# Kernel tuning notes

Measured on AMD Instinct MI355X. Metric: run time of the kernel, lower is better.

## Reference

```python
import jax, jax.numpy as jnp
import numpy as np

# dims: batch, nodes, d_node, d_edge, d_attn_hid, heads, d_node_hid, d_edge_hid, layers
B, N, DN, DE, DH, H, DNH, DEH, L = 2, 256, 128, 64, 128, 8, 512, 256, 2
DHH = DH // H  # per-head dim
SCALE = 1.0 / (DH ** 0.5)  # source scales by full d_hid, not per-head dim


def _ln(x, g, b):
    m = jnp.mean(x, -1, keepdims=True)
    v = jnp.mean((x - m) ** 2, -1, keepdims=True)
    return (x - m) * jax.lax.rsqrt(v + 1e-5) * g + b


def _gelu(x):
    return jax.nn.gelu(x, approximate=False)  # torch nn.GELU default = exact erf


def setup_inputs() -> dict:
    key = jax.random.key(0)
    ks = iter(jax.random.split(key, 40))
    def w(shape, scale=0.02):
        return jax.random.normal(next(ks), shape, jnp.float32) * scale
    return {
        "node_features": jax.random.normal(next(ks), (B, N, DN), jnp.float32),
        "edge_features": jax.random.normal(next(ks), (B, N, N, DE), jnp.float32),
        "Wqkv_n": w((L, DN, 3 * DH)),
        "Wqkv_e": w((L, DE, 4 * DH)),
        "Wo": w((L, DH, DN)), "bo": jnp.zeros((L, DN), jnp.float32),
        "Wl0": w((L, DN, DN)), "bl0": jnp.zeros((L, DN), jnp.float32),
        "ln0_g": jnp.ones((L, DN), jnp.float32), "ln0_b": jnp.zeros((L, DN), jnp.float32),
        "Wm1": w((L, DN, DNH)), "Wm2": w((L, DNH, DN)), "bm2": jnp.zeros((L, DN), jnp.float32),
        "ln1_g": jnp.ones((L, DN), jnp.float32), "ln1_b": jnp.zeros((L, DN), jnp.float32),
        "We0": w((L, 2 * DE, DEH)), "be0": jnp.zeros((L, DEH), jnp.float32),
        "Ws": w((L, DN, DEH)), "bs": jnp.zeros((L, DEH), jnp.float32),
        "Wt": w((L, DN, DEH)), "bt": jnp.zeros((L, DEH), jnp.float32),
        "We1": w((L, DEH, DE)), "be1": jnp.zeros((L, DE), jnp.float32),
        "eln0_g": jnp.ones((L, DE), jnp.float32), "eln0_b": jnp.zeros((L, DE), jnp.float32),
        "Wem1": w((L, DE, DEH)), "Wem2": w((L, DEH, DE)), "bem2": jnp.zeros((L, DE), jnp.float32),
        "eln1_g": jnp.ones((L, DE), jnp.float32), "eln1_b": jnp.zeros((L, DE), jnp.float32),
    }


def _forward(node_features, edge_features, Wqkv_n, Wqkv_e, Wo, bo, Wl0, bl0,
             ln0_g, ln0_b, Wm1, Wm2, bm2, ln1_g, ln1_b, We0, be0, Ws, bs, Wt, bt,
             We1, be1, eln0_g, eln0_b, Wem1, Wem2, bem2, eln1_g, eln1_b):
    x, e = node_features, edge_features
    for l in range(L):
        # --- RTAttention (modulate_v=True, eval mode) ---
        qkv_n = (x @ Wqkv_n[l]).reshape(B, N, H, 3 * DHH).transpose(0, 2, 1, 3)  # b h n 3d
        qn, kn, vn = jnp.split(qkv_n, 3, axis=-1)
        qkv_e = (e @ Wqkv_e[l]).reshape(B, N, N, H, 4 * DHH).transpose(0, 3, 1, 2, 4)  # b h i j 4d
        eq, ek, ev, em = jnp.split(qkv_e, 4, axis=-1)
        q = qn[:, :, :, None, :] + eq            # b h i j d
        k = kn[:, :, None, :, :] + ek            # b h i j d
        v = vn[:, :, None, :, :] * em + ev       # modulated values
        dots = SCALE * jnp.einsum('bhijd,bhijd->bhij', q, k)
        attn = jax.nn.softmax(dots, axis=-1)
        out = jnp.einsum('bhij,bhijd->bhid', attn, v)
        out = out.transpose(0, 2, 1, 3).reshape(B, N, DH)
        attn_out = out @ Wo[l] + bo[l]
        # --- node updates: ln(x + lin0(attn)); ln(x + mlp(x)) ---
        x = _ln(x + (attn_out @ Wl0[l] + bl0[l]), ln0_g[l], ln0_b[l])
        x = _ln(x + (_gelu(x @ Wm1[l]) @ Wm2[l] + bm2[l]), ln1_g[l], ln1_b[l])
        # --- edge updates (EdgeLayer) ---
        src = (x @ Ws[l] + bs[l])[:, :, None, :]   # broadcast over target j
        tgt = (x @ Wt[l] + bt[l])[:, None, :, :]   # broadcast over source i
        ecat = jnp.concatenate([e, e.transpose(0, 2, 1, 3)], axis=-1)  # [e_ij, e_ji]
        h = _gelu(ecat @ We0[l] + be0[l] + src + tgt)
        e = _ln(e + (h @ We1[l] + be1[l]), eln0_g[l], eln0_b[l])
        e = _ln(e + (_gelu(e @ Wem1[l]) @ Wem2[l] + bem2[l]), eln1_g[l], eln1_b[l])
    return x, e


def reference(node_features, edge_features, Wqkv_n, Wqkv_e, Wo, bo, Wl0, bl0,
              ln0_g, ln0_b, Wm1, Wm2, bm2, ln1_g, ln1_b, We0, be0, Ws, bs, Wt, bt,
              We1, be1, eln0_g, eln0_b, Wem1, Wem2, bem2, eln1_g, eln1_b):
    return _forward(node_features, edge_features, Wqkv_n, Wqkv_e, Wo, bo, Wl0, bl0,
                    ln0_g, ln0_b, Wm1, Wm2, bm2, ln1_g, ln1_b, We0, be0, Ws, bs, Wt, bt,
                    We1, be1, eln0_g, eln0_b, Wem1, Wem2, bem2, eln1_g, eln1_b)
```

## Files before the change

### kernel.cpp

```cpp
#include <hip/hip_runtime.h>
#include <hip/hip_bf16.h>
#include <stdint.h>

#define BB 2
#define NN 256
#define DN 128
#define DE 64
#define DH 128
#define NH 8
#define DHH 16
#define DNH 512
#define DEH 256
#define NL 2
#define SCALE_ATT 0.08838834764831845f

typedef __hip_bfloat16 bf16;
typedef __attribute__((ext_vector_type(8))) short short8;
typedef __attribute__((ext_vector_type(4))) float f32x4;

__device__ __forceinline__ float gelu_f(float x) {
  return 0.5f * x * (1.0f + erff(x * 0.70710678118654752f));
}
__device__ __forceinline__ float gelu_t(float x) {
  float m2u = x * fmaf(x * x, -0.07135481627f, -1.59576912161f);
  float e = __expf(m2u);
  return x * __builtin_amdgcn_rcpf(1.f + e);
}

template <int ctrl>
__device__ __forceinline__ float dppf(float v) {
  return __int_as_float(
      __builtin_amdgcn_update_dpp(0, __float_as_int(v), ctrl, 0xF, 0xF, true));
}
__device__ __forceinline__ float row_sum16(float v) {
  v += dppf<0xB1>(v);
  v += dppf<0x4E>(v);
  v += dppf<0x124>(v);
  v += dppf<0x128>(v);
  return v;
}
__device__ __forceinline__ float row_max16(float v) {
  v = fmaxf(v, dppf<0xB1>(v));
  v = fmaxf(v, dppf<0x4E>(v));
  v = fmaxf(v, dppf<0x124>(v));
  v = fmaxf(v, dppf<0x128>(v));
  return v;
}
__device__ __forceinline__ float wave_sum(float v) {
  v = row_sum16(v);
  v += __shfl_xor(v, 16, 64);
  v += __shfl_xor(v, 32, 64);
  return v;
}
__device__ __forceinline__ float wave_max(float v) {
  v = row_max16(v);
  v = fmaxf(v, __shfl_xor(v, 16, 64));
  v = fmaxf(v, __shfl_xor(v, 32, 64));
  return v;
}

__device__ __forceinline__ short f2bf(float f) {
  union { float f; uint32_t u; } v{f};
  uint32_t r = (v.u + 0x7FFFu + ((v.u >> 16) & 1u)) >> 16;
  return (short)r;
}
__device__ __forceinline__ float bf2f(short s) {
  union { uint32_t u; float f; } v;
  v.u = ((uint32_t)(uint16_t)s) << 16;
  return v.f;
}

__global__ void k_detect(const uint32_t* g8, const uint32_t* g13, int* flag) {
  if (threadIdx.x == 0 && blockIdx.x == 0) {
    uint32_t a = g8[0], b = g13[0];
    *flag = (a == 0x3F803F80u || b == 0x3F803F80u) ? 1 : 0;
  }
}

struct CastArgs {
  const void* src[30];
  float* dst[30];
  int n[30];
  const int* flag;
};

__global__ __launch_bounds__(256) void k_cast_all(CastArgs a) {
  int ti = blockIdx.y;
  float* d = a.dst[ti];
  int n = a.n[ti];
  int stride = gridDim.x * blockDim.x;
  if (*a.flag) {
    const bf16* s = (const bf16*)a.src[ti];
    for (int i = blockIdx.x * blockDim.x + threadIdx.x; i < n; i += stride)
      d[i] = __bfloat162float(s[i]);
  } else {
    const float* s = (const float*)a.src[ti];
    for (int i = blockIdx.x * blockDim.x + threadIdx.x; i < n; i += stride)
      d[i] = s[i];
  }
}

__global__ __launch_bounds__(256) void k_cast_e(const void* __restrict__ src,
                                                short* __restrict__ dst,
                                                const int* __restrict__ flag) {
  const int n8 = BB * NN * NN * DE / 8;
  int stride = gridDim.x * blockDim.x;
  if (*flag) {
    const uint4* s = (const uint4*)src;
    uint4* d = (uint4*)dst;
    for (int i = blockIdx.x * blockDim.x + threadIdx.x; i < n8; i += stride) d[i] = s[i];
  } else {
    const float4* s = (const float4*)src;
    for (int i = blockIdx.x * blockDim.x + threadIdx.x; i < n8; i += stride) {
      float4 a = s[2 * i], b = s[2 * i + 1];
      short* o = dst + 8 * i;
      o[0] = f2bf(a.x); o[1] = f2bf(a.y); o[2] = f2bf(a.z); o[3] = f2bf(a.w);
      o[4] = f2bf(b.x); o[5] = f2bf(b.y); o[6] = f2bf(b.z); o[7] = f2bf(b.w);
    }
  }
}

__global__ __launch_bounds__(256) void k_cast_out(const float* __restrict__ x,
                                                  const short* __restrict__ e,
                                                  void* __restrict__ out_v,
                                                  const int* __restrict__ flag) {
  const int nx = BB * NN * DN;
  const int total = nx + BB * NN * NN * DE;
  int stride = gridDim.x * blockDim.x;
  if (*flag) {
    short* out = (short*)out_v;
    for (int i = blockIdx.x * blockDim.x + threadIdx.x; i < total; i += stride)
      out[i] = (i < nx) ? f2bf(x[i]) : e[i - nx];
  } else {
    float* out = (float*)out_v;
    for (int i = blockIdx.x * blockDim.x + threadIdx.x; i < total; i += stride)
      out[i] = (i < nx) ? x[i] : bf2f(e[i - nx]);
  }
}

struct WtJob { const float* src; short* dst; int K; int N; };
struct WtArgs { WtJob job[10]; };
__global__ __launch_bounds__(256) void k_wtrans_all(WtArgs a) {
  WtJob j = a.job[blockIdx.y];
  int total = j.K * j.N;
  int stride = gridDim.x * 256;
  for (int idx = blockIdx.x * 256 + threadIdx.x; idx < total; idx += stride) {
    int k = idx / j.N, n = idx - k * j.N;
    j.dst[n * j.K + k] = f2bf(j.src[idx]);
  }
}

__global__ __launch_bounds__(128) void k_node_qkv(const float* __restrict__ x,
                                                  const float* __restrict__ W,
                                                  float* __restrict__ qkv) {
  int row = blockIdx.x;
  __shared__ float xs[DN];
  int t = threadIdx.x;
  xs[t] = x[row * DN + t];
  __syncthreads();
#pragma unroll
  for (int c0 = 0; c0 < 384; c0 += 128) {
    int c = c0 + t;
    float a = 0.f;
    for (int k = 0; k < DN; ++k) a = fmaf(xs[k], W[k * 384 + c], a);
    qkv[row * 384 + c] = a;
  }
}

__global__ __launch_bounds__(256) void k_attn_node(
    const short* __restrict__ e, const short* __restrict__ WqeT,
    const float* __restrict__ qkv_in,
    const float* __restrict__ Wo, const float* __restrict__ bo,
    const float* __restrict__ Wl0, const float* __restrict__ bl0,
    const float* __restrict__ g0, const float* __restrict__ b0n,
    const float* __restrict__ Wm1, const float* __restrict__ Wm2,
    const float* __restrict__ bm2, const float* __restrict__ g1,
    const float* __restrict__ b1n, const float* __restrict__ Ws,
    const float* __restrict__ bs, const float* __restrict__ Wt,
    const float* __restrict__ bt, const float* __restrict__ WqnN,
    float* __restrict__ qkv_out, float* __restrict__ srcb,
    float* __restrict__ tgtb, float* __restrict__ x) {
  int i = blockIdx.x, b = blockIdx.y;
  int row = b * NN + i;
  __shared__ short est[256 * 72];
  __shared__ float sp[NH * NN];
  __shared__ float qnl[DH];
  __shared__ float osh[DH];
  __shared__ float t1s[DH];
  __shared__ float xs[DN];
  __shared__ float hsb[DNH];
  __shared__ float part[256];
  __shared__ float red[4];
  int t = threadIdx.x;
  for (int idx = t; idx < 2048; idx += 256) {
    int j = idx >> 3, c8 = (idx & 7) * 8;
    *(short8*)(est + j * 72 + c8) =
        *(const short8*)(e + ((size_t)(b * NN + i) * NN + j) * DE + c8);
  }
  if (t < DH) qnl[t] = qkv_in[(size_t)row * 384 + (t >> 4) * 48 + (t & 15)];
  __syncthreads();

  int wv = t >> 6, lane = t & 63, g8 = lane >> 4, lo = lane & 15;

  {
    short8 bq[2][2][2];
#pragma unroll
    for (int hh = 0; hh < 2; ++hh)
#pragma unroll
      for (int p = 0; p < 2; ++p)
#pragma unroll
        for (int ks = 0; ks < 2; ++ks)
          bq[hh][p][ks] = *(const short8*)(
              WqeT + (size_t)(((wv * 2 + hh) * 4 + p) * 16 + lo) * 64 + ks * 32 + g8 * 8);
    for (int mt = 0; mt < 16; ++mt) {
      short8 a0 = *(const short8*)(est + (mt * 16 + lo) * 72 + g8 * 8);
      short8 a1 = *(const short8*)(est + (mt * 16 + lo) * 72 + 32 + g8 * 8);
#pragma unroll
      for (int hh = 0; hh < 2; ++hh) {
        int h = wv * 2 + hh;
        float kn4[4];
#pragma unroll
        for (int r = 0; r < 4; ++r)
          kn4[r] = qkv_in[(size_t)(b * NN + mt * 16 + g8 * 4 + r) * 384 + h * 48 + 16 + lo];
        f32x4 cq = {0.f, 0.f, 0.f, 0.f}, ck = {0.f, 0.f, 0.f, 0.f};
        cq = __builtin_amdgcn_mfma_f32_16x16x32_bf16(a0, bq[hh][0][0], cq, 0, 0, 0);
        cq = __builtin_amdgcn_mfma_f32_16x16x32_bf16(a1, bq[hh][0][1], cq, 0, 0, 0);
        ck = __builtin_amdgcn_mfma_f32_16x16x32_bf16(a0, bq[hh][1][0], ck, 0, 0, 0);
        ck = __builtin_amdgcn_mfma_f32_16x16x32_bf16(a1, bq[hh][1][1], ck, 0, 0, 0);
        float qv = qnl[h * 16 + lo];
#pragma unroll
        for (int r = 0; r < 4; ++r) {
          int j = mt * 16 + g8 * 4 + r;
          float s = (qv + cq[r]) * (kn4[r] + ck[r]);
          s = row_sum16(s);
          if (lo == 0) sp[h * NN + j] = s * SCALE_ATT;
        }
      }
    }
  }
  __syncthreads();

#pragma unroll
  for (int hh = 0; hh < 2; ++hh) {
    int h = wv * 2 + hh;
    float v[4];
#pragma unroll
    for (int q = 0; q < 4; ++q) v[q] = sp[h * NN + lane + 64 * q];
    float m = fmaxf(fmaxf(v[0], v[1]), fmaxf(v[2], v[3]));
    m = wave_max(m);
    float l = 0.f;
#pragma unroll
    for (int q = 0; q < 4; ++q) { v[q] = __expf(v[q] - m); l += v[q]; }
    l = wave_sum(l);
    float inv = 1.f / l;
#pragma unroll
    for (int q = 0; q < 4; ++q) sp[h * NN + lane + 64 * q] = v[q] * inv;
  }
  __syncthreads();

  {
    short8 bv[2][2][2];
#pragma unroll
    for (int hh = 0; hh < 2; ++hh)
#pragma unroll
      for (int p = 0; p < 2; ++p)
#pragma unroll
        for (int ks = 0; ks < 2; ++ks)
          bv[hh][p][ks] = *(const short8*)(
              WqeT + (size_t)(((wv * 2 + hh) * 4 + 2 + p) * 16 + lo) * 64 + ks * 32 + g8 * 8);
    float oacc[2] = {0.f, 0.f};
    for (int mt = 0; mt < 16; ++mt) {
      short8 a0 = *(const short8*)(est + (mt * 16 + lo) * 72 + g8 * 8);
      short8 a1 = *(const short8*)(est + (mt * 16 + lo) * 72 + 32 + g8 * 8);
#pragma unroll
      for (int hh = 0; hh < 2; ++hh) {
        int h = wv * 2 + hh;
        float vn4[4];
#pragma unroll
        for (int r = 0; r < 4; ++r)
          vn4[r] = qkv_in[(size_t)(b * NN + mt * 16 + g8 * 4 + r) * 384 + h * 48 + 32 + lo];
        f32x4 cv = {0.f, 0.f, 0.f, 0.f}, cm = {0.f, 0.f, 0.f, 0.f};
        cv = __builtin_amdgcn_mfma_f32_16x16x32_bf16(a0, bv[hh][0][0], cv, 0, 0, 0);
        cv = __builtin_amdgcn_mfma_f32_16x16x32_bf16(a1, bv[hh][0][1], cv, 0, 0, 0);
        cm = __builtin_amdgcn_mfma_f32_16x16x32_bf16(a0, bv[hh][1][0], cm, 0, 0, 0);
        cm = __builtin_amdgcn_mfma_f32_16x16x32_bf16(a1, bv[hh][1][1], cm, 0, 0, 0);
#pragma unroll
        for (int r = 0; r < 4; ++r) {
          int j = mt * 16 + g8 * 4 + r;
          float vv = fmaf(vn4[r], cm[r], cv[r]);
          oacc[hh] = fmaf(sp[h * NN + j], vv, oacc[hh]);
        }
      }
    }
#pragma unroll
    for (int hh = 0; hh < 2; ++hh) {
      int h = wv * 2 + hh;
      float o = oacc[hh];
      o += __shfl_xor(o, 16, 64);
      o += __shfl_xor(o, 32, 64);
      if (g8 == 0) osh[h * 16 + lo] = o;
    }
  }
  __syncthreads();

  int col = t & 127, kh = t >> 7;
  {
    float a = 0.f;
    int k0 = kh * 64;
    for (int k = k0; k < k0 + 64; ++k) a = fmaf(osh[k], Wo[k * DN + col], a);
    part[t] = a;
  }
  __syncthreads();
  if (t < DH) t1s[t] = part[t] + part[t + 128] + bo[t];
  __syncthreads();
  {
    float a = 0.f;
    int k0 = kh * 64;
    for (int k = k0; k < k0 + 64; ++k) a = fmaf(t1s[k], Wl0[k * DN + col], a);
    part[t] = a;
  }
  __syncthreads();
  if (t < DN) {
    float y = part[t] + part[t + 128] + bl0[t] + x[(size_t)row * DN + t];
    float s1 = wave_sum(y), s2 = wave_sum(y * y);
    if ((t & 63) == 0) { red[t >> 6] = s1; red[2 + (t >> 6)] = s2; }
    part[t] = y;
  }
  __syncthreads();
  if (t < DN) {
    float y = part[t];
    float mean = (red[0] + red[1]) * (1.f / 128.f);
    float var = (red[2] + red[3]) * (1.f / 128.f) - mean * mean;
    float rr = rsqrtf(var + 1e-5f);
    xs[t] = (y - mean) * rr * g0[t] + b0n[t];
  }
  __syncthreads();
#pragma unroll
  for (int p = 0; p < 2; ++p) {
    int c = t + 256 * p;
    float a = 0.f;
    for (int k = 0; k < DN; ++k) a = fmaf(xs[k], Wm1[k * DNH + c], a);
    hsb[c] = gelu_f(a);
  }
  __syncthreads();
  {
    float a = 0.f;
    int k0 = kh * 256;
    for (int k = k0; k < k0 + 256; ++k) a = fmaf(hsb[k], Wm2[k * DN + col], a);
    part[t] = a;
  }
  __syncthreads();
  if (t < DN) {
    float y = part[t] + part[t + 128] + bm2[t] + xs[t];
    float s1 = wave_sum(y), s2 = wave_sum(y * y);
    if ((t & 63) == 0) { red[t >> 6] = s1; red[2 + (t >> 6)] = s2; }
    part[t] = y;
  }
  __syncthreads();
  if (t < DN) {
    float y = part[t];
    float mean = (red[0] + red[1]) * (1.f / 128.f);
    float var = (red[2] + red[3]) * (1.f / 128.f) - mean * mean;
    float rr = rsqrtf(var + 1e-5f);
    float x2 = (y - mean) * rr * g1[t] + b1n[t];
    x[(size_t)row * DN + t] = x2;
    xs[t] = x2;
  }
  __syncthreads();
  {
    float a = bs[t], cc = bt[t];
    for (int k = 0; k < DN; ++k) {
      float xv = xs[k];
      a = fmaf(xv, Ws[k * DEH + t], a);
      cc = fmaf(xv, Wt[k * DEH + t], cc);
    }
    srcb[(size_t)row * DEH + t] = a;
    tgtb[(size_t)row * DEH + t] = cc;
  }
  if (WqnN) {
#pragma unroll
    for (int p = 0; p < 2; ++p) {
      int c = t + 256 * p;
      if (c < 384) {
        float a = 0.f;
        for (int k = 0; k < DN; ++k) a = fmaf(xs[k], WqnN[k * 384 + c], a);
        qkv_out[(size_t)row * 384 + c] = a;
      }
    }
  }
}

__global__ __launch_bounds__(256) void k_edge_fused(
    const short* __restrict__ e_in, const short* __restrict__ W0T,
    const float* __restrict__ b0, const short* __restrict__ W1T,
    const float* __restrict__ b1, const float* __restrict__ srcb,
    const float* __restrict__ tgtb, const float* __restrict__ g,
    const float* __restrict__ bb, const short* __restrict__ Wm1T,
    const short* __restrict__ Wm2T, const float* __restrict__ bm2,
    const float* __restrict__ gm, const float* __restrict__ bbm,
    short* __restrict__ e_out) {
  int bid = blockIdx.x;
  int swz = (bid & 7) * 256 + (bid >> 3);
  int jt = swz & 3, i = (swz >> 2) & 255, b = swz >> 10;
  int j0 = jt * 64;
  __shared__ short hidT[64 * 264];
  int t = threadIdx.x;
  int wv = t >> 6, lane = t & 63, g8 = lane >> 4, lo = lane & 15;
  int nq = wv * 64;
  int m0 = wv * 16;

  {
    float bias_n[4];
#pragma unroll
    for (int nt = 0; nt < 4; ++nt)
      bias_n[nt] = b0[nq + nt * 16 + lo] + srcb[(size_t)(b * NN + i) * DEH + nq + nt * 16 + lo];
    short8 bfr1[4][4];
#pragma unroll
    for (int nt = 0; nt < 4; ++nt)
#pragma unroll
      for (int ks = 0; ks < 4; ++ks)
        bfr1[nt][ks] =
            *(const short8*)(W0T + (size_t)(nq + nt * 16 + lo) * 128 + ks * 32 + g8 * 8);
#pragma unroll
    for (int mt = 0; mt < 4; ++mt) {
      int mrow = mt * 16 + lo;
      float tg[4][4];
#pragma unroll
      for (int nt = 0; nt < 4; ++nt)
#pragma unroll
        for (int r = 0; r < 4; ++r)
          tg[nt][r] = tgtb[((size_t)(b * NN) + j0 + mt * 16 + g8 * 4 + r) * DEH +
                           nq + nt * 16 + lo];
      short8 a[4];
      const short* eA = e_in + ((size_t)(b * NN + i) * NN + j0 + mrow) * DE;
#pragma unroll
      for (int ks = 0; ks < 2; ++ks) a[ks] = *(const short8*)(eA + ks * 32 + g8 * 8);
      const short* eT = e_in + ((size_t)(b * NN + j0 + mrow) * NN + i) * DE;
#pragma unroll
      for (int ks = 0; ks < 2; ++ks) a[2 + ks] = *(const short8*)(eT + ks * 32 + g8 * 8);
      f32x4 acc[4];
#pragma unroll
      for (int nt = 0; nt < 4; ++nt) {
        f32x4 c = {0.f, 0.f, 0.f, 0.f};
#pragma unroll
        for (int ks = 0; ks < 4; ++ks)
          c = __builtin_amdgcn_mfma_f32_16x16x32_bf16(a[ks], bfr1[nt][ks], c, 0, 0, 0);
        acc[nt] = c;
      }
#pragma unroll
      for (int nt = 0; nt < 4; ++nt) {
        int n = nq + nt * 16 + lo;
#pragma unroll
        for (int r = 0; r < 4; ++r) {
          int m = mt * 16 + g8 * 4 + r;
          hidT[m * 264 + n] = f2bf(gelu_t(acc[nt][r] + bias_n[nt] + tg[nt][r]));
        }
      }
    }
  }
  float resv[4][4];
#pragma unroll
  for (int nt = 0; nt < 4; ++nt)
#pragma unroll
    for (int r = 0; r < 4; ++r)
      resv[nt][r] = bf2f(e_in[((size_t)(b * NN + i) * NN + j0 + m0 + g8 * 4 + r) * DE +
                              nt * 16 + lo]);
  __syncthreads();

  float emid[4][4];
  {
    short8 a2[8];
#pragma unroll
    for (int ks = 0; ks < 8; ++ks)
      a2[ks] = *(const short8*)(hidT + (m0 + lo) * 264 + ks * 32 + g8 * 8);
    f32x4 acc2[4];
#pragma unroll
    for (int nt = 0; nt < 4; ++nt) {
      f32x4 c = {0.f, 0.f, 0.f, 0.f};
      const short* bp = W1T + (size_t)(nt * 16 + lo) * 256;
#pragma unroll
      for (int ks = 0; ks < 8; ++ks)
        c = __builtin_amdgcn_mfma_f32_16x16x32_bf16(
            a2[ks], *(const short8*)(bp + ks * 32 + g8 * 8), c, 0, 0, 0);
      acc2[nt] = c;
    }
#pragma unroll
    for (int nt = 0; nt < 4; ++nt) {
      int n = nt * 16 + lo;
      float bb1 = b1[n];
#pragma unroll
      for (int r = 0; r < 4; ++r) emid[nt][r] = acc2[nt][r] + bb1 + resv[nt][r];
    }
#pragma unroll
    for (int r = 0; r < 4; ++r) {
      float s = emid[0][r] + emid[1][r] + emid[2][r] + emid[3][r];
      float q = emid[0][r] * emid[0][r] + emid[1][r] * emid[1][r] +
                emid[2][r] * emid[2][r] + emid[3][r] * emid[3][r];
      s = row_sum16(s);
      q = row_sum16(q);
      float mean = s * (1.f / 64.f);
      float var = q * (1.f / 64.f) - mean * mean;
      float rr = rsqrtf(var + 1e-5f);
      int m = m0 + g8 * 4 + r;
#pragma unroll
      for (int nt = 0; nt < 4; ++nt) {
        int n = nt * 16 + lo;
        float v = (emid[nt][r] - mean) * rr * g[n] + bb[n];
        emid[nt][r] = v;
        hidT[m * 264 + n] = f2bf(v);
      }
    }
  }

  {
    short8 a3[2];
#pragma unroll
    for (int ks = 0; ks < 2; ++ks)
      a3[ks] = *(const short8*)(hidT + (m0 + lo) * 264 + ks * 32 + g8 * 8);
#pragma unroll 4
    for (int nt = 0; nt < 16; ++nt) {
      f32x4 c = {0.f, 0.f, 0.f, 0.f};
      const short* bp = Wm1T + (size_t)(nt * 16 + lo) * 64;
#pragma unroll
      for (int ks = 0; ks < 2; ++ks)
        c = __builtin_amdgcn_mfma_f32_16x16x32_bf16(
            a3[ks], *(const short8*)(bp + ks * 32 + g8 * 8), c, 0, 0, 0);
      int n = nt * 16 + lo;
#pragma unroll
      for (int r = 0; r < 4; ++r)
        hidT[(m0 + g8 * 4 + r) * 264 + n] = f2bf(gelu_t(c[r]));
    }
  }

  {
    short8 a4[8];
#pragma unroll
    for (int ks = 0; ks < 8; ++ks)
      a4[ks] = *(const short8*)(hidT + (m0 + lo) * 264 + ks * 32 + g8 * 8);
    f32x4 acc4[4];
#pragma unroll
    for (int nt = 0; nt < 4; ++nt) {
      f32x4 c = {0.f, 0.f, 0.f, 0.f};
      const short* bp = Wm2T + (size_t)(nt * 16 + lo) * 256;
#pragma unroll
      for (int ks = 0; ks < 8; ++ks)
        c = __builtin_amdgcn_mfma_f32_16x16x32_bf16(
            a4[ks], *(const short8*)(bp + ks * 32 + g8 * 8), c, 0, 0, 0);
      acc4[nt] = c;
    }
    float vals[4][4];
#pragma unroll
    for (int nt = 0; nt < 4; ++nt) {
      int n = nt * 16 + lo;
      float bv = bm2[n];
#pragma unroll
      for (int r = 0; r < 4; ++r) vals[nt][r] = acc4[nt][r] + bv + emid[nt][r];
    }
#pragma unroll
    for (int r = 0; r < 4; ++r) {
      float s = vals[0][r] + vals[1][r] + vals[2][r] + vals[3][r];
      float q = vals[0][r] * vals[0][r] + vals[1][r] * vals[1][r] +
                vals[2][r] * vals[2][r] + vals[3][r] * vals[3][r];
      s = row_sum16(s);
      q = row_sum16(q);
      float mean = s * (1.f / 64.f);
      float var = q * (1.f / 64.f) - mean * mean;
      float rr = rsqrtf(var + 1e-5f);
      int m = m0 + g8 * 4 + r;
#pragma unroll
      for (int nt = 0; nt < 4; ++nt) {
        int n = nt * 16 + lo;
        e_out[((size_t)(b * NN + i) * NN + j0 + m) * DE + n] =
            f2bf((vals[nt][r] - mean) * rr * gm[n] + bbm[n]);
      }
    }
  }
}

extern "C" void kernel_launch(void* const* d_in, const int* in_sizes, int n_in,
                              void* d_out, int out_size, void* d_ws, size_t ws_size,
                              hipStream_t stream) {
  float* ws = (float*)d_ws;
  int* flag = (int*)ws;
  size_t off = 64;
  auto alloc = [&](size_t n) {
    float* p = ws + off;
    off += (n + 63) & ~(size_t)63;
    return p;
  };
  float* x_f = alloc((size_t)BB * NN * DN);
  short* e_a = (short*)alloc((size_t)BB * NN * NN * DE / 2);
  short* e_b = (short*)alloc((size_t)BB * NN * NN * DE / 2);
  float* qkv = alloc((size_t)BB * NN * 384);
  float* srcb = alloc((size_t)BB * NN * DEH);
  float* tgtb = alloc((size_t)BB * NN * DEH);
  short* WqeT = (short*)alloc(NL * 512 * 64 / 2);
  short* We0T = (short*)alloc(NL * 256 * 128 / 2);
  short* We1T = (short*)alloc(NL * 64 * 256 / 2);
  short* Wem1T = (short*)alloc(NL * 256 * 64 / 2);
  short* Wem2T = (short*)alloc(NL * 64 * 256 / 2);

  float* wf[30];
  wf[0] = x_f;
  wf[1] = x_f;
  CastArgs ca;
  int ntens = n_in < 30 ? n_in : 30;
  for (int idx = 0; idx < ntens; ++idx) {
    if (idx >= 2) wf[idx] = alloc((size_t)in_sizes[idx]);
    ca.src[idx] = d_in[idx];
    ca.dst[idx] = wf[idx];
    ca.n[idx] = (idx == 1) ? 0 : in_sizes[idx];
  }
  ca.flag = flag;

  k_detect<<<1, 64, 0, stream>>>((const uint32_t*)d_in[8], (const uint32_t*)d_in[13], flag);
  k_cast_all<<<dim3(64, ntens), dim3(256), 0, stream>>>(ca);
  k_cast_e<<<1024, 256, 0, stream>>>(d_in[1], e_a, flag);
  WtArgs wa;
  for (int l = 0; l < NL; ++l) {
    wa.job[l * 5 + 0] = {wf[3] + (size_t)l * DE * 512, WqeT + (size_t)l * 512 * 64, DE, 512};
    wa.job[l * 5 + 1] = {wf[15] + (size_t)l * 128 * 256, We0T + (size_t)l * 256 * 128, 128, 256};
    wa.job[l * 5 + 2] = {wf[21] + (size_t)l * 256 * 64, We1T + (size_t)l * 64 * 256, 256, 64};
    wa.job[l * 5 + 3] = {wf[25] + (size_t)l * 64 * 256, Wem1T + (size_t)l * 256 * 64, 64, 256};
    wa.job[l * 5 + 4] = {wf[26] + (size_t)l * 64 * 256, Wem2T + (size_t)l * 64 * 256, 256, 64};
  }
  k_wtrans_all<<<dim3(64, 10), 256, 0, stream>>>(wa);

  k_node_qkv<<<BB * NN, 128, 0, stream>>>(x_f, wf[2], qkv);

  for (int l = 0; l < NL; ++l) {
    const float* Wo = wf[4] + (size_t)l * DH * DN;
    const float* bo = wf[5] + (size_t)l * DN;
    const float* Wl0 = wf[6] + (size_t)l * DN * DN;
    const float* bl0 = wf[7] + (size_t)l * DN;
    const float* g0 = wf[8] + (size_t)l * DN;
    const float* b0n = wf[9] + (size_t)l * DN;
    const float* Wm1 = wf[10] + (size_t)l * DN * DNH;
    const float* Wm2 = wf[11] + (size_t)l * DNH * DN;
    const float* bm2 = wf[12] + (size_t)l * DN;
    const float* g1 = wf[13] + (size_t)l * DN;
    const float* b1n = wf[14] + (size_t)l * DN;
    const float* be0 = wf[16] + (size_t)l * DEH;
    const float* Wsw = wf[17] + (size_t)l * DN * DEH;
    const float* bsw = wf[18] + (size_t)l * DEH;
    const float* Wtw = wf[19] + (size_t)l * DN * DEH;
    const float* btw = wf[20] + (size_t)l * DEH;
    const float* be1 = wf[22] + (size_t)l * DE;
    const float* eg0 = wf[23] + (size_t)l * DE;
    const float* eb0 = wf[24] + (size_t)l * DE;
    const float* bem2 = wf[27] + (size_t)l * DE;
    const float* eg1 = wf[28] + (size_t)l * DE;
    const float* eb1 = wf[29] + (size_t)l * DE;
    const float* WqnNext = (l + 1 < NL) ? (wf[2] + (size_t)(l + 1) * DN * 3 * DH) : nullptr;

    const short* e_cur = (l == 0) ? e_a : e_b;
    short* e_nxt = (l == 0) ? e_b : e_a;

    k_attn_node<<<dim3(NN, BB), 256, 0, stream>>>(
        e_cur, WqeT + (size_t)l * 512 * 64, qkv,
        Wo, bo, Wl0, bl0, g0, b0n, Wm1, Wm2, bm2, g1, b1n,
        Wsw, bsw, Wtw, btw, WqnNext, qkv, srcb, tgtb, x_f);
    k_edge_fused<<<dim3(NN / 64 * NN * BB), 256, 0, stream>>>(
        e_cur, We0T + (size_t)l * 256 * 128, be0, We1T + (size_t)l * 64 * 256, be1,
        srcb, tgtb, eg0, eb0,
        Wem1T + (size_t)l * 256 * 64, Wem2T + (size_t)l * 64 * 256, bem2, eg1, eb1,
        e_nxt);
  }
  k_cast_out<<<1024, 256, 0, stream>>>(x_f, e_a, d_out, flag);
}
```

Baseline: 550.8 us.

## Double k_attn_node block to 512 threads, one wave per attention head

Raises the attention/node kernel from 256 to 512 threads so each of the 8 waves handles a single head rather than two. The later node matvecs get split four ways along K, with the partial sums reduced through a larger shared buffer, and the src/tgt projections are spread across all threads. The aim is more parallelism per row block, since the grid holds only 512 blocks, shortening each block's serial critical path. The cost is higher register pressure under the 512-thread launch bound and extra reduction traffic through shared memory.

```diff
diff --git a/kernel.cpp b/kernel.cpp
--- a/kernel.cpp
+++ b/kernel.cpp
@@ -167,7 +167,7 @@
   }
 }
 
-__global__ __launch_bounds__(256) void k_attn_node(
+__global__ __launch_bounds__(512) void k_attn_node(
     const short* __restrict__ e, const short* __restrict__ WqeT,
     const float* __restrict__ qkv_in,
     const float* __restrict__ Wo, const float* __restrict__ bo,
@@ -189,10 +189,10 @@
   __shared__ float t1s[DH];
   __shared__ float xs[DN];
   __shared__ float hsb[DNH];
-  __shared__ float part[256];
+  __shared__ float part[512];
   __shared__ float red[4];
   int t = threadIdx.x;
-  for (int idx = t; idx < 2048; idx += 256) {
+  for (int idx = t; idx < 2048; idx += 512) {
     int j = idx >> 3, c8 = (idx & 7) * 8;
     *(short8*)(est + j * 72 + c8) =
         *(const short8*)(e + ((size_t)(b * NN + i) * NN + j) * DE + c8);
@@ -201,48 +201,41 @@
   __syncthreads();
 
   int wv = t >> 6, lane = t & 63, g8 = lane >> 4, lo = lane & 15;
-
-  {
-    short8 bq[2][2][2];
-#pragma unroll
-    for (int hh = 0; hh < 2; ++hh)
-#pragma unroll
-      for (int p = 0; p < 2; ++p)
-#pragma unroll
-        for (int ks = 0; ks < 2; ++ks)
-          bq[hh][p][ks] = *(const short8*)(
-              WqeT + (size_t)(((wv * 2 + hh) * 4 + p) * 16 + lo) * 64 + ks * 32 + g8 * 8);
+  int h = wv;
+
+  {
+    short8 bq[2][2];
+#pragma unroll
+    for (int p = 0; p < 2; ++p)
+#pragma unroll
+      for (int ks = 0; ks < 2; ++ks)
+        bq[p][ks] = *(const short8*)(
+            WqeT + (size_t)((h * 4 + p) * 16 + lo) * 64 + ks * 32 + g8 * 8);
+    float qv = qnl[h * 16 + lo];
     for (int mt = 0; mt < 16; ++mt) {
       short8 a0 = *(const short8*)(est + (mt * 16 + lo) * 72 + g8 * 8);
       short8 a1 = *(const short8*)(est + (mt * 16 + lo) * 72 + 32 + g8 * 8);
-#pragma unroll
-      for (int hh = 0; hh < 2; ++hh) {
-        int h = wv * 2 + hh;
-        float kn4[4];
-#pragma unroll
-        for (int r = 0; r < 4; ++r)
-          kn4[r] = qkv_in[(size_t)(b * NN + mt * 16 + g8 * 4 + r) * 384 + h * 48 + 16 + lo];
-        f32x4 cq = {0.f, 0.f, 0.f, 0.f}, ck = {0.f, 0.f, 0.f, 0.f};
-        cq = __builtin_amdgcn_mfma_f32_16x16x32_bf16(a0, bq[hh][0][0], cq, 0, 0, 0);
-        cq = __builtin_amdgcn_mfma_f32_16x16x32_bf16(a1, bq[hh][0][1], cq, 0, 0, 0);
-        ck = __builtin_amdgcn_mfma_f32_16x16x32_bf16(a0, bq[hh][1][0], ck, 0, 0, 0);
-        ck = __builtin_amdgcn_mfma_f32_16x16x32_bf16(a1, bq[hh][1][1], ck, 0, 0, 0);
-        float qv = qnl[h * 16 + lo];
-#pragma unroll
-        for (int r = 0; r < 4; ++r) {
-          int j = mt * 16 + g8 * 4 + r;
-          float s = (qv + cq[r]) * (kn4[r] + ck[r]);
-          s = row_sum16(s);
-          if (lo == 0) sp[h * NN + j] = s * SCALE_ATT;
-        }
+      float kn4[4];
+#pragma unroll
+      for (int r = 0; r < 4; ++r)
+        kn4[r] = qkv_in[(size_t)(b * NN + mt * 16 + g8 * 4 + r) * 384 + h * 48 + 16 + lo];
+      f32x4 cq = {0.f, 0.f, 0.f, 0.f}, ck = {0.f, 0.f, 0.f, 0.f};
+      cq = __builtin_amdgcn_mfma_f32_16x16x32_bf16(a0, bq[0][0], cq, 0, 0, 0);
+      cq = __builtin_amdgcn_mfma_f32_16x16x32_bf16(a1, bq[0][1], cq, 0, 0, 0);
+      ck = __builtin_amdgcn_mfma_f32_16x16x32_bf16(a0, bq[1][0], ck, 0, 0, 0);
+      ck = __builtin_amdgcn_mfma_f32_16x16x32_bf16(a1, bq[1][1], ck, 0, 0, 0);
+#pragma unroll
+      for (int r = 0; r < 4; ++r) {
+        int j = mt * 16 + g8 * 4 + r;
+        float s = (qv + cq[r]) * (kn4[r] + ck[r]);
+        s = row_sum16(s);
+        if (lo == 0) sp[h * NN + j] = s * SCALE_ATT;
       }
     }
   }
   __syncthreads();
 
-#pragma unroll
-  for (int hh = 0; hh < 2; ++hh) {
-    int h = wv * 2 + hh;
+  {
     float v[4];
 #pragma unroll
     for (int q = 0; q < 4; ++q) v[q] = sp[h * NN + lane + 64 * q];
@@ -259,69 +252,60 @@
   __syncthreads();
 
   {
-    short8 bv[2][2][2];
-#pragma unroll
-    for (int hh = 0; hh < 2; ++hh)
-#pragma unroll
-      for (int p = 0; p < 2; ++p)
-#pragma unroll
-        for (int ks = 0; ks < 2; ++ks)
-          bv[hh][p][ks] = *(const short8*)(
-              WqeT + (size_t)(((wv * 2 + hh) * 4 + 2 + p) * 16 + lo) * 64 + ks * 32 + g8 * 8);
-    float oacc[2] = {0.f, 0.f};
+    short8 bv[2][2];
+#pragma unroll
+    for (int p = 0; p < 2; ++p)
+#pragma unroll
+      for (int ks = 0; ks < 2; ++ks)
+        bv[p][ks] = *(const short8*)(
+            WqeT + (size_t)((h * 4 + 2 + p) * 16 + lo) * 64 + ks * 32 + g8 * 8);
+    float oacc = 0.f;
     for (int mt = 0; mt < 16; ++mt) {
       short8 a0 = *(const short8*)(est + (mt * 16 + lo) * 72 + g8 * 8);
       short8 a1 = *(const short8*)(est + (mt * 16 + lo) * 72 + 32 + g8 * 8);
-#pragma unroll
-      for (int hh = 0; hh < 2; ++hh) {
-        int h = wv * 2 + hh;
-        float vn4[4];
-#pragma unroll
-        for (int r = 0; r < 4; ++r)
-          vn4[r] = qkv_in[(size_t)(b * NN + mt * 16 + g8 * 4 + r) * 384 + h * 48 + 32 + lo];
-        f32x4 cv = {0.f, 0.f, 0.f, 0.f}, cm = {0.f, 0.f, 0.f, 0.f};
-        cv = __builtin_amdgcn_mfma_f32_16x16x32_bf16(a0, bv[hh][0][0], cv, 0, 0, 0);
-        cv = __builtin_amdgcn_mfma_f32_16x16x32_bf16(a1, bv[hh][0][1], cv, 0, 0, 0);
-        cm = __builtin_amdgcn_mfma_f32_16x16x32_bf16(a0, bv[hh][1][0], cm, 0, 0, 0);
-        cm = __builtin_amdgcn_mfma_f32_16x16x32_bf16(a1, bv[hh][1][1], cm, 0, 0, 0);
-#pragma unroll
-        for (int r = 0; r < 4; ++r) {
-          int j = mt * 16 + g8 * 4 + r;
-          float vv = fmaf(vn4[r], cm[r], cv[r]);
-          oacc[hh] = fmaf(sp[h * NN + j], vv, oacc[hh]);
-        }
+      float vn4[4];
+#pragma unroll
+      for (int r = 0; r < 4; ++r)
+        vn4[r] = qkv_in[(size_t)(b * NN + mt * 16 + g8 * 4 + r) * 384 + h * 48 + 32 + lo];
+      f32x4 cv = {0.f, 0.f, 0.f, 0.f}, cm = {0.f, 0.f, 0.f, 0.f};
+      cv = __builtin_amdgcn_mfma_f32_16x16x32_bf16(a0, bv[0][0], cv, 0, 0, 0);
+      cv = __builtin_amdgcn_mfma_f32_16x16x32_bf16(a1, bv[0][1], cv, 0, 0, 0);
+      cm = __builtin_amdgcn_mfma_f32_16x16x32_bf16(a0, bv[1][0], cm, 0, 0, 0);
+      cm = __builtin_amdgcn_mfma_f32_16x16x32_bf16(a1, bv[1][1], cm, 0, 0, 0);
+#pragma unroll
+      for (int r = 0; r < 4; ++r) {
+        int j = mt * 16 + g8 * 4 + r;
+        float vv = fmaf(vn4[r], cm[r], cv[r]);
+        oacc = fmaf(sp[h * NN + j], vv, oacc);
       }
     }
-#pragma unroll
-    for (int hh = 0; hh < 2; ++hh) {
-      int h = wv * 2 + hh;
-      float o = oacc[hh];
-      o += __shfl_xor(o, 16, 64);
-      o += __shfl_xor(o, 32, 64);
-      if (g8 == 0) osh[h * 16 + lo] = o;
-    }
-  }
-  __syncthreads();
-
-  int col = t & 127, kh = t >> 7;
+    oacc += __shfl_xor(oacc, 16, 64);
+    oacc += __shfl_xor(oacc, 32, 64);
+    if (g8 == 0) osh[h * 16 + lo] = oacc;
+  }
+  __syncthreads();
+
+  int col = t & 127, kq = t >> 7;
   {
     float a = 0.f;
-    int k0 = kh * 64;
-    for (int k = k0; k < k0 + 64; ++k) a = fmaf(osh[k], Wo[k * DN + col], a);
+    int k0 = kq * 32;
+    for (int k = k0; k < k0 + 32; ++k) a = fmaf(osh[k], Wo[k * DN + col], a);
     part[t] = a;
   }
   __syncthreads();
-  if (t < DH) t1s[t] = part[t] + part[t + 128] + bo[t];
+  if (t < DH)
+    t1s[t] = part[t] + part[t + 128] + part[t + 256] + part[t + 384] + bo[t];
   __syncthreads();
   {
     float a = 0.f;
-    int k0 = kh * 64;
-    for (int k = k0; k < k0 + 64; ++k) a = fmaf(t1s[k], Wl0[k * DN + col], a);
+    int k0 = kq * 32;
+    for (int k = k0; k < k0 + 32; ++k) a = fmaf(t1s[k], Wl0[k * DN + col], a);
     part[t] = a;
   }
   __syncthreads();
   if (t < DN) {
-    float y = part[t] + part[t + 128] + bl0[t] + x[(size_t)row * DN + t];
+    float y = part[t] + part[t + 128] + part[t + 256] + part[t + 384] +
+              bl0[t] + x[(size_t)row * DN + t];
     float s1 = wave_sum(y), s2 = wave_sum(y * y);
     if ((t & 63) == 0) { red[t >> 6] = s1; red[2 + (t >> 6)] = s2; }
     part[t] = y;
@@ -335,23 +319,22 @@
     xs[t] = (y - mean) * rr * g0[t] + b0n[t];
   }
   __syncthreads();
-#pragma unroll
-  for (int p = 0; p < 2; ++p) {
-    int c = t + 256 * p;
+  {
     float a = 0.f;
-    for (int k = 0; k < DN; ++k) a = fmaf(xs[k], Wm1[k * DNH + c], a);
-    hsb[c] = gelu_f(a);
+    for (int k = 0; k < DN; ++k) a = fmaf(xs[k], Wm1[k * DNH + t], a);
+    hsb[t] = gelu_f(a);
   }
   __syncthreads();
   {
     float a = 0.f;
-    int k0 = kh * 256;
-    for (int k = k0; k < k0 + 256; ++k) a = fmaf(hsb[k], Wm2[k * DN + col], a);
+    int k0 = kq * 128;
+    for (int k = k0; k < k0 + 128; ++k) a = fmaf(hsb[k], Wm2[k * DN + col], a);
     part[t] = a;
   }
   __syncthreads();
   if (t < DN) {
-    float y = part[t] + part[t + 128] + bm2[t] + xs[t];
+    float y = part[t] + part[t + 128] + part[t + 256] + part[t + 384] +
+              bm2[t] + xs[t];
     float s1 = wave_sum(y), s2 = wave_sum(y * y);
     if ((t & 63) == 0) { red[t >> 6] = s1; red[2 + (t >> 6)] = s2; }
     part[t] = y;
@@ -368,25 +351,17 @@
   }
   __syncthreads();
   {
-    float a = bs[t], cc = bt[t];
-    for (int k = 0; k < DN; ++k) {
-      float xv = xs[k];
-      a = fmaf(xv, Ws[k * DEH + t], a);
-      cc = fmaf(xv, Wt[k * DEH + t], cc);
-    }
-    srcb[(size_t)row * DEH + t] = a;
-    tgtb[(size_t)row * DEH + t] = cc;
-  }
-  if (WqnN) {
-#pragma unroll
-    for (int p = 0; p < 2; ++p) {
-      int c = t + 256 * p;
-      if (c < 384) {
-        float a = 0.f;
-        for (int k = 0; k < DN; ++k) a = fmaf(xs[k], WqnN[k * 384 + c], a);
-        qkv_out[(size_t)row * 384 + c] = a;
-      }
-    }
+    int c = t & 255;
+    bool issrc = t < 256;
+    const float* W = issrc ? Ws : Wt;
+    float a = issrc ? bs[c] : bt[c];
+    for (int k = 0; k < DN; ++k) a = fmaf(xs[k], W[k * DEH + c], a);
+    (issrc ? srcb : tgtb)[(size_t)row * DEH + c] = a;
+  }
+  if (WqnN && t < 384) {
+    float a = 0.f;
+    for (int k = 0; k < DN; ++k) a = fmaf(xs[k], WqnN[k * 384 + t], a);
+    qkv_out[(size_t)row * 384 + t] = a;
   }
 }
 
@@ -656,7 +631,7 @@
     const short* e_cur = (l == 0) ? e_a : e_b;
     short* e_nxt = (l == 0) ? e_b : e_a;
 
-    k_attn_node<<<dim3(NN, BB), 256, 0, stream>>>(
+    k_attn_node<<<dim3(NN, BB), 512, 0, stream>>>(
         e_cur, WqeT + (size_t)l * 512 * 64, qkv,
         Wo, bo, Wl0, bl0, g0, b0n, Wm1, Wm2, bm2, g1, b1n,
         Wsw, bsw, Wtw, btw, WqnNext, qkv, srcb, tgtb, x_f);
```

Result: slower. 568.6 us (+3.2%).
